# Optimization experiments

Measured on AMD Instinct MI355X. Metric: run time of the kernel, lower is better.

## Reference

```python
import jax, jax.numpy as jnp
import numpy as np

NUM_HEADS = 12
KEEP_RATE = 0.7
EPS = 1e-5  # torch nn.LayerNorm default


def layernorm(x, w, b):
    m = x.mean(-1, keepdims=True)
    v = ((x - m) ** 2).mean(-1, keepdims=True)
    return (x - m) * jax.lax.rsqrt(v + EPS) * w + b


def complement_idx(idx, dim):
    # idx: (B, L) top-k indices into [0, dim). Returns (B, dim-L) sorted complement,
    # matching EViT's scatter-zeros-then-sort trick.
    a = jnp.broadcast_to(jnp.arange(dim, dtype=idx.dtype), idx.shape[:-1] + (dim,))
    masked = jax.vmap(lambda ar, ix: ar.at[ix].set(0))(a, idx)
    n_idx = idx.shape[-1]
    return jnp.sort(masked, axis=-1)[..., n_idx:]


def setup_inputs() -> dict:
    key = jax.random.key(0)
    ks = jax.random.split(key, 8)
    B, N, C = 128, 197, 768
    H = 4 * C
    std = 0.02
    return {
        "x": jax.random.normal(ks[0], (B, N, C), jnp.float32),
        "norm1_w": jnp.ones((C,), jnp.float32),
        "norm1_b": jnp.zeros((C,), jnp.float32),
        "qkv_w": jax.random.normal(ks[1], (C, 3 * C), jnp.float32) * std,  # qkv_bias=False
        "proj_w": jax.random.normal(ks[2], (C, C), jnp.float32) * std,
        "proj_b": jnp.zeros((C,), jnp.float32),
        "norm2_w": jnp.ones((C,), jnp.float32),
        "norm2_b": jnp.zeros((C,), jnp.float32),
        "fc1_w": jax.random.normal(ks[3], (C, H), jnp.float32) * std,
        "fc1_b": jnp.zeros((H,), jnp.float32),
        "fc2_w": jax.random.normal(ks[4], (H, C), jnp.float32) * std,
        "fc2_b": jnp.zeros((C,), jnp.float32),
    }


def reference(x, norm1_w, norm1_b, qkv_w, proj_w, proj_b,
              norm2_w, norm2_b, fc1_w, fc1_b, fc2_w, fc2_b):
    B, N, C = x.shape
    h = NUM_HEADS
    d = C // h
    scale = d ** -0.5

    # ---- Attention (eval mode, no dropout) ----
    xn = layernorm(x, norm1_w, norm1_b)
    qkv = (xn @ qkv_w).reshape(B, N, 3, h, d).transpose(2, 0, 3, 1, 4)
    q, k, v = qkv[0], qkv[1], qkv[2]  # (B, h, N, d)
    attn = jax.nn.softmax(jnp.einsum('bhqd,bhkd->bhqk', q, k) * scale, axis=-1)
    out = jnp.einsum('bhqk,bhkd->bhqd', attn, v).transpose(0, 2, 1, 3).reshape(B, N, C)
    x = x + (out @ proj_w + proj_b)

    # ---- Top-k token selection (keep_rate < 1) ----
    left = int(np.ceil(KEEP_RATE * (N - 1)))          # 138 kept patch tokens
    cls_attn = attn[:, :, 0, 1:].mean(axis=1)         # (B, N-1)
    _, idx = jax.lax.top_k(cls_attn, left)            # sorted descending, like torch.topk
    compl = complement_idx(idx, N - 1)                # (B, M), M = N-1-left

    non_cls = x[:, 1:]                                # (B, N-1, C)
    gather = lambda arr, ix: jnp.take_along_axis(arr, ix[..., None], axis=1)

    x_others = gather(non_cls, idx)                   # (B, L, C)
    non_topk = gather(non_cls, compl)                 # (B, M, C)
    xo_n = x_others / jnp.linalg.norm(x_others, axis=-1, keepdims=True)
    nt_n = non_topk / jnp.linalg.norm(non_topk, axis=-1, keepdims=True)
    distance = jnp.einsum('bmc,blc->bml', nt_n, xo_n)  # cosine similarity (B, M, L)

    # attention-weighted merge of pruned tokens into nearest kept token
    non_cls_w = non_cls * cls_attn[..., None]
    x_others = gather(non_cls_w, idx)
    non_topk = gather(non_cls_w, compl)
    topk_attn = jnp.take_along_axis(cls_attn, idx, axis=1)       # (B, L)
    non_topk_attn = jnp.take_along_axis(cls_attn, compl, axis=1)  # (B, M)
    node_idx = jnp.argmax(distance, axis=-1)                      # (B, M)

    topk_attn = jax.vmap(lambda t, ni, nt: t.at[ni].add(nt))(topk_attn, node_idx, non_topk_attn)
    x_others = jax.vmap(lambda xo, ni, nt: xo.at[ni].add(nt))(x_others, node_idx, non_topk)
    x_others = x_others / topk_attn[..., None]

    x = jnp.concatenate([x[:, :1], x_others], axis=1)  # (B, L+1, C)

    # ---- MLP ----
    xn2 = layernorm(x, norm2_w, norm2_b)
    hmid = jax.nn.gelu(xn2 @ fc1_w + fc1_b, approximate=False)
    x = x + (hmid @ fc2_w + fc2_b)
    return x
```

## Files before the change

### kernel.cpp

```cpp
#include <hip/hip_runtime.h>
#include <math.h>

#define B_ 128
#define N_ 197
#define C_ 768
#define H_ 12
#define D_ 64
#define KEEP_ 138
#define COMP_ 58
#define NOUT_ 139
#define HID_ 3072

typedef __attribute__((ext_vector_type(8))) short bf16x8;
typedef __attribute__((ext_vector_type(8))) _Float16 f16x8;
typedef __attribute__((ext_vector_type(4))) float f32x4;
typedef unsigned short us;

__device__ inline us f2bf(float f) {
    unsigned u = __float_as_uint(f);
    unsigned r = (u + 0x7FFFu + ((u >> 16) & 1u)) >> 16;
    return (us)r;
}
__device__ inline float bf2f(us h) { return __uint_as_float(((unsigned)h) << 16); }
__device__ inline void gload_lds16(const void* g, void* l) {
    __builtin_amdgcn_global_load_lds((const __attribute__((address_space(1))) void*)g,
                                     (__attribute__((address_space(3))) void*)l, 16, 0, 0);
}
__device__ inline void split3(float v, us& h1, us& h2, us& h3) {
    h1 = f2bf(v);
    float r1 = v - bf2f(h1);
    h2 = f2bf(r1);
    h3 = f2bf(r1 - bf2f(h2));
}
__device__ inline void split2h(float v, us& h1, us& h2) {
    float av = fabsf(v);
    float v1 = (av < 6.103515625e-05f) ? 0.f : v;
    _Float16 a = (_Float16)v1;
    float r = (v - (float)a) * 4096.0f;
    _Float16 b = (_Float16)r;
    h1 = *reinterpret_cast<us*>(&a);
    h2 = *reinterpret_cast<us*>(&b);
}

__device__ inline float fast_gelu(float v) {
    float x = v * 0.70710678118654752f;
    float ax = fabsf(x);
    float t = __frcp_rn(__fmaf_rn(0.3275911f, ax, 1.0f));
    float p = __fmaf_rn(1.061405429f, t, -1.453152027f);
    p = __fmaf_rn(p, t, 1.421413741f);
    p = __fmaf_rn(p, t, -0.284496736f);
    p = __fmaf_rn(p, t, 0.254829592f);
    p = p * t;
    float e = __expf(-x * x);
    float erfa = __fmaf_rn(-p, e, 1.0f);
    float er = (x < 0.f) ? -erfa : erfa;
    return 0.5f * v * (1.0f + er);
}

#define WAITV(n) asm volatile("s_waitcnt vmcnt(" #n ")" ::: "memory")
#define RBAR __builtin_amdgcn_s_barrier()

__global__ __launch_bounds__(256) void ln_split2h_kernel(const float* __restrict__ x,
                                                         const float* __restrict__ w,
                                                         const float* __restrict__ bias,
                                                         us* __restrict__ y1,
                                                         us* __restrict__ y2) {
    int row = blockIdx.x;
    const float* xr = x + (size_t)row * C_;
    int tid = threadIdx.x;
    float v[3];
    float s = 0.f, sq = 0.f;
#pragma unroll
    for (int i = 0; i < 3; i++) {
        v[i] = xr[tid + i * 256];
        s += v[i];
        sq += v[i] * v[i];
    }
    __shared__ float s1[256], s2[256];
    s1[tid] = s; s2[tid] = sq;
    __syncthreads();
    for (int o = 128; o > 0; o >>= 1) {
        if (tid < o) { s1[tid] += s1[tid + o]; s2[tid] += s2[tid + o]; }
        __syncthreads();
    }
    float mean = s1[0] * (1.0f / C_);
    float var = s2[0] * (1.0f / C_) - mean * mean;
    float rstd = rsqrtf(var + 1e-5f);
#pragma unroll
    for (int i = 0; i < 3; i++) {
        int c = tid + i * 256;
        float y = (v[i] - mean) * rstd * w[c] + bias[c];
        us h1, h2;
        split2h(y, h1, h2);
        size_t o = (size_t)row * C_ + c;
        y1[o] = h1; y2[o] = h2;
    }
}

__global__ __launch_bounds__(256) void ln2bf_kernel(const float* __restrict__ x,
                                                    const float* __restrict__ w,
                                                    const float* __restrict__ bias,
                                                    us* __restrict__ y) {
    int row = blockIdx.x;
    const float* xr = x + (size_t)row * C_;
    us* yr = y + (size_t)row * C_;
    int tid = threadIdx.x;
    float v[3];
    float s = 0.f, sq = 0.f;
#pragma unroll
    for (int i = 0; i < 3; i++) {
        v[i] = xr[tid + i * 256];
        s += v[i];
        sq += v[i] * v[i];
    }
    __shared__ float s1[256], s2[256];
    s1[tid] = s; s2[tid] = sq;
    __syncthreads();
    for (int o = 128; o > 0; o >>= 1) {
        if (tid < o) { s1[tid] += s1[tid + o]; s2[tid] += s2[tid + o]; }
        __syncthreads();
    }
    float mean = s1[0] * (1.0f / C_);
    float var = s2[0] * (1.0f / C_) - mean * mean;
    float rstd = rsqrtf(var + 1e-5f);
#pragma unroll
    for (int i = 0; i < 3; i++) {
        int c = tid + i * 256;
        yr[c] = f2bf((v[i] - mean) * rstd * w[c] + bias[c]);
    }
}

__global__ __launch_bounds__(256) void wtrans_kernel(const float* __restrict__ in,
                                                     us* __restrict__ out,
                                                     int K, int N) {
    __shared__ float T[32][33];
    int n0 = blockIdx.x * 32, k0 = blockIdx.y * 32;
    int tx = threadIdx.x & 31, ty = threadIdx.x >> 5;
    for (int i = 0; i < 32; i += 8)
        T[ty + i][tx] = in[(size_t)(k0 + ty + i) * N + n0 + tx];
    __syncthreads();
    for (int i = 0; i < 32; i += 8)
        out[(size_t)(n0 + ty + i) * K + k0 + tx] = f2bf(T[tx][ty + i]);
}

__global__ __launch_bounds__(256) void wtrans_split2h_kernel(const float* __restrict__ in,
                                                             us* __restrict__ o1,
                                                             us* __restrict__ o2,
                                                             int K, int N) {
    __shared__ float T[32][33];
    int n0 = blockIdx.x * 32, k0 = blockIdx.y * 32;
    int tx = threadIdx.x & 31, ty = threadIdx.x >> 5;
    for (int i = 0; i < 32; i += 8)
        T[ty + i][tx] = in[(size_t)(k0 + ty + i) * N + n0 + tx];
    __syncthreads();
    for (int i = 0; i < 32; i += 8) {
        us h1, h2;
        split2h(T[tx][ty + i], h1, h2);
        size_t o = (size_t)(n0 + ty + i) * K + k0 + tx;
        o1[o] = h1; o2[o] = h2;
    }
}

template <bool BIAS, bool RES>
__global__ __launch_bounds__(256, 2) void bgemm3h_kernel(const us* __restrict__ A1,
                                                         const us* __restrict__ A2,
                                                         const us* __restrict__ B1,
                                                         const us* __restrict__ B2,
                                                         const float* __restrict__ bias,
                                                         const float* __restrict__ res,
                                                         float* __restrict__ Cm,
                                                         int M, int N, int K) {
    __shared__ short As[2][128 * 64];
    __shared__ short Bs[2][128 * 64];
    int tid = threadIdx.x;
    int lane = tid & 63, wid = tid >> 6;
    int wr = wid >> 1, wc = wid & 1;
    int lr = lane & 15, g = lane >> 4;
    int brow = blockIdx.y * 128, bcol = blockIdx.x * 128;

    f32x4 acc0[4][4] = {};
    f32x4 acc1[4][4] = {};

    for (int k0 = 0; k0 < K; k0 += 64) {
#pragma unroll
        for (int v = 0; v < 4; v++) {
            int rowb = v * 32 + wid * 8;
            int r = rowb + (lane >> 3);
            int slot = lane & 7;
            int chunk = slot ^ (r & 7);
            int garow = brow + r; if (garow >= M) garow = M - 1;
            int gbrow = bcol + r;
            gload_lds16(A1 + (size_t)garow * K + k0 + chunk * 8, &As[0][rowb * 64]);
            gload_lds16(A2 + (size_t)garow * K + k0 + chunk * 8, &As[1][rowb * 64]);
            gload_lds16(B1 + (size_t)gbrow * K + k0 + chunk * 8, &Bs[0][rowb * 64]);
            gload_lds16(B2 + (size_t)gbrow * K + k0 + chunk * 8, &Bs[1][rowb * 64]);
        }
        __syncthreads();
#pragma unroll
        for (int kk = 0; kk < 2; kk++) {
            f16x8 af[2][4], bfr[2][4];
#pragma unroll
            for (int fi = 0; fi < 4; fi++) {
                int ra = wr * 64 + fi * 16 + lr;
                int sla = (kk * 4 + g) ^ (ra & 7);
                int rb = wc * 64 + fi * 16 + lr;
                int slb = (kk * 4 + g) ^ (rb & 7);
#pragma unroll
                for (int s = 0; s < 2; s++) {
                    af[s][fi] = *reinterpret_cast<const f16x8*>(&As[s][ra * 64 + sla * 8]);
                    bfr[s][fi] = *reinterpret_cast<const f16x8*>(&Bs[s][rb * 64 + slb * 8]);
                }
            }
#pragma unroll
            for (int fi = 0; fi < 4; fi++)
#pragma unroll
                for (int fj = 0; fj < 4; fj++) {
                    acc0[fi][fj] = __builtin_amdgcn_mfma_f32_16x16x32_f16(af[0][fi], bfr[0][fj], acc0[fi][fj], 0, 0, 0);
                    acc1[fi][fj] = __builtin_amdgcn_mfma_f32_16x16x32_f16(af[0][fi], bfr[1][fj], acc1[fi][fj], 0, 0, 0);
                    acc1[fi][fj] = __builtin_amdgcn_mfma_f32_16x16x32_f16(af[1][fi], bfr[0][fj], acc1[fi][fj], 0, 0, 0);
                }
        }
        __syncthreads();
    }
#pragma unroll
    for (int fi = 0; fi < 4; fi++) {
#pragma unroll
        for (int fj = 0; fj < 4; fj++) {
            int col = bcol + wc * 64 + fj * 16 + lr;
            float bv = BIAS ? bias[col] : 0.f;
#pragma unroll
            for (int i = 0; i < 4; i++) {
                int r = brow + wr * 64 + fi * 16 + g * 4 + i;
                if (r < M) {
                    float vv = acc0[fi][fj][i] + acc1[fi][fj][i] * (1.0f / 4096.0f) + bv;
                    if (RES) vv += res[(size_t)r * N + col];
                    Cm[(size_t)r * N + col] = vv;
                }
            }
        }
    }
}

template <bool GELU_, bool OUTBF, bool RES>
__global__ __launch_bounds__(256, 4) void bgemm_kernel(const us* __restrict__ A,
                                                       const us* __restrict__ Bt,
                                                       const float* __restrict__ bias,
                                                       const float* __restrict__ res,
                                                       void* __restrict__ Cout,
                                                       int M, int N, int K) {
    __shared__ short As0[128 * 32];
    __shared__ short Bs0[128 * 32];
    __shared__ short As1[128 * 32];
    __shared__ short Bs1[128 * 32];
    int tid = threadIdx.x;
    int lane = tid & 63, wid = tid >> 6;
    int wr = wid >> 1, wc = wid & 1;
    int lr = lane & 15, g = lane >> 4;
    int brow = blockIdx.y * 128, bcol = blockIdx.x * 128;
    int lrow = lane >> 2, lslot = lane & 3;
    const int sa = (g ^ ((lr >> 1) & 3)) * 8;

    f32x4 acc[4][4] = {};

    auto stage = [&](short (&Aa)[128 * 32], short (&Bb)[128 * 32], int k0) {
#pragma unroll
        for (int v = 0; v < 2; v++) {
            int rowb = wid * 32 + v * 16;
            int ra = rowb + lrow;
            int hsel = (lslot ^ ((lrow >> 1) & 3)) * 8;
            int garow = brow + ra; if (garow >= M) garow = M - 1;
            gload_lds16(A + (size_t)garow * K + k0 + hsel, &Aa[rowb * 32]);
            gload_lds16(Bt + (size_t)(bcol + ra) * K + k0 + hsel, &Bb[rowb * 32]);
        }
    };
    auto compute = [&](short (&Aa)[128 * 32], short (&Bb)[128 * 32]) {
        bf16x8 af[4], bfr[4];
#pragma unroll
        for (int fi = 0; fi < 4; fi++)
            af[fi] = *reinterpret_cast<const bf16x8*>(&Aa[(wr * 64 + fi * 16 + lr) * 32 + sa]);
#pragma unroll
        for (int fj = 0; fj < 4; fj++)
            bfr[fj] = *reinterpret_cast<const bf16x8*>(&Bb[(wc * 64 + fj * 16 + lr) * 32 + sa]);
#pragma unroll
        for (int fi = 0; fi < 4; fi++)
#pragma unroll
            for (int fj = 0; fj < 4; fj++)
                acc[fi][fj] = __builtin_amdgcn_mfma_f32_16x16x32_bf16(af[fi], bfr[fj], acc[fi][fj], 0, 0, 0);
    };

    stage(As0, Bs0, 0);
    for (int k0 = 0; k0 < K; k0 += 64) {
        if (k0 + 32 < K) {
            stage(As1, Bs1, k0 + 32);
            WAITV(4);
        } else {
            WAITV(0);
        }
        RBAR;
        compute(As0, Bs0);
        RBAR;
        if (k0 + 64 < K) {
            stage(As0, Bs0, k0 + 64);
            WAITV(4);
        } else {
            WAITV(0);
        }
        RBAR;
        compute(As1, Bs1);
        RBAR;
    }
#pragma unroll
    for (int fi = 0; fi < 4; fi++) {
#pragma unroll
        for (int fj = 0; fj < 4; fj++) {
            int col = bcol + wc * 64 + fj * 16 + lr;
            float bv = bias[col];
#pragma unroll
            for (int i = 0; i < 4; i++) {
                int r = brow + wr * 64 + fi * 16 + g * 4 + i;
                if (r < M) {
                    float vv = acc[fi][fj][i] + bv;
                    if (GELU_) vv = fast_gelu(vv);
                    if (OUTBF) {
                        ((us*)Cout)[(size_t)r * N + col] = f2bf(vv);
                    } else {
                        if (RES) vv += res[(size_t)r * N + col];
                        ((float*)Cout)[(size_t)r * N + col] = vv;
                    }
                }
            }
        }
    }
}

__global__ __launch_bounds__(512, 1) void attn11_kernel(const float* __restrict__ qkv,
                                                        us* __restrict__ ao1,
                                                        us* __restrict__ ao2,
                                                        float* __restrict__ attn0,
                                                        int b0) {
    int hh = blockIdx.x, b = blockIdx.y;
    int tid = threadIdx.x, lane = tid & 63, wv = tid >> 6;
    int lr = lane & 15, g = lane >> 4;
    __shared__ short Ks[3][208 * 64];
    __shared__ short Vt[2][64 * 224];
    __shared__ unsigned Pscr[8][16 * 32];
    const size_t base = (size_t)b * N_ * 3 * C_ + (size_t)hh * D_;

    for (int i = tid; i < 208 * 8; i += 512) {
        int k = i >> 3, oct = i & 7;
        int d0 = (oct ^ (k & 7)) * 8;
        float tv[8];
        if (k < N_) {
            const float4* kp = reinterpret_cast<const float4*>(qkv + base + (size_t)k * 3 * C_ + C_ + d0);
            float4 aa = kp[0], bb = kp[1];
            tv[0] = aa.x; tv[1] = aa.y; tv[2] = aa.z; tv[3] = aa.w;
            tv[4] = bb.x; tv[5] = bb.y; tv[6] = bb.z; tv[7] = bb.w;
        } else {
#pragma unroll
            for (int e = 0; e < 8; e++) tv[e] = 0.f;
        }
        bf16x8 h1v, h2v, h3v;
#pragma unroll
        for (int e = 0; e < 8; e++) {
            us ha, hb, hc;
            split3(tv[e], ha, hb, hc);
            h1v[e] = (short)ha; h2v[e] = (short)hb; h3v[e] = (short)hc;
        }
        int di = k * 64 + oct * 8;
        *reinterpret_cast<bf16x8*>(&Ks[0][di]) = h1v;
        *reinterpret_cast<bf16x8*>(&Ks[1][di]) = h2v;
        *reinterpret_cast<bf16x8*>(&Ks[2][di]) = h3v;
    }
    {
        int d = tid & 63, jb = tid >> 6;
        for (int it = 0; it < 28; it++) {
            int k = it * 8 + jb;
            float vv = (k < N_) ? qkv[base + (size_t)k * 3 * C_ + 2 * C_ + d] : 0.f;
            us p1 = f2bf(vv);
            us p2 = f2bf(vv - bf2f(p1));
            int idx = d * 224 + (((k >> 3) ^ (d & 3)) * 8) + (k & 7);
            Vt[0][idx] = (short)p1;
            Vt[1][idx] = (short)p2;
        }
    }
    __syncthreads();

#pragma unroll
    for (int chunk = 0; chunk < 2; chunk++) {
        int qbase = chunk * 128 + wv * 16;
        bf16x8 qf1[2], qf2[2], qf3[2];
        int qrow = qbase + lr;
#pragma unroll
        for (int kk = 0; kk < 2; kk++) {
            float qv[8];
            if (qrow < N_) {
                const float4* qp = reinterpret_cast<const float4*>(qkv + base + (size_t)qrow * 3 * C_ + kk * 32 + g * 8);
                float4 aa = qp[0], bb = qp[1];
                qv[0] = aa.x; qv[1] = aa.y; qv[2] = aa.z; qv[3] = aa.w;
                qv[4] = bb.x; qv[5] = bb.y; qv[6] = bb.z; qv[7] = bb.w;
            } else {
#pragma unroll
                for (int e = 0; e < 8; e++) qv[e] = 0.f;
            }
#pragma unroll
            for (int e = 0; e < 8; e++) {
                us ha, hb, hc;
                split3(qv[e], ha, hb, hc);
                qf1[kk][e] = (short)ha; qf2[kk][e] = (short)hb; qf3[kk][e] = (short)hc;
            }
        }
        f32x4 sacc[13] = {};
#pragma unroll
        for (int kt = 0; kt < 13; kt++) {
#pragma unroll
            for (int kk = 0; kk < 2; kk++) {
                int row = kt * 16 + lr;
                int sl = ((kk * 4 + g) ^ (row & 7)) * 8;
                const bf16x8 b1 = *reinterpret_cast<const bf16x8*>(&Ks[0][row * 64 + sl]);
                const bf16x8 b2 = *reinterpret_cast<const bf16x8*>(&Ks[1][row * 64 + sl]);
                const bf16x8 b3 = *reinterpret_cast<const bf16x8*>(&Ks[2][row * 64 + sl]);
                sacc[kt] = __builtin_amdgcn_mfma_f32_16x16x32_bf16(qf1[kk], b1, sacc[kt], 0, 0, 0);
                sacc[kt] = __builtin_amdgcn_mfma_f32_16x16x32_bf16(qf1[kk], b2, sacc[kt], 0, 0, 0);
                sacc[kt] = __builtin_amdgcn_mfma_f32_16x16x32_bf16(qf2[kk], b1, sacc[kt], 0, 0, 0);
                sacc[kt] = __builtin_amdgcn_mfma_f32_16x16x32_bf16(qf1[kk], b3, sacc[kt], 0, 0, 0);
                sacc[kt] = __builtin_amdgcn_mfma_f32_16x16x32_bf16(qf3[kk], b1, sacc[kt], 0, 0, 0);
                sacc[kt] = __builtin_amdgcn_mfma_f32_16x16x32_bf16(qf2[kk], b2, sacc[kt], 0, 0, 0);
            }
        }
#pragma unroll
        for (int i = 0; i < 4; i++) {
            float m = -1e30f;
#pragma unroll
            for (int kt = 0; kt < 13; kt++) {
                int k = kt * 16 + lr;
                float lgv = (k < N_) ? sacc[kt][i] * 0.125f : -1e30f;
                sacc[kt][i] = lgv;
                m = fmaxf(m, lgv);
            }
            m = fmaxf(m, __shfl_xor(m, 1, 64));
            m = fmaxf(m, __shfl_xor(m, 2, 64));
            m = fmaxf(m, __shfl_xor(m, 4, 64));
            m = fmaxf(m, __shfl_xor(m, 8, 64));
            float se = 0.f;
#pragma unroll
            for (int kt = 0; kt < 13; kt++) {
                int k = kt * 16 + lr;
                float e = (k < N_) ? expf(sacc[kt][i] - m) : 0.f;
                sacc[kt][i] = e;
                se += e;
            }
            se += __shfl_xor(se, 1, 64);
            se += __shfl_xor(se, 2, 64);
            se += __shfl_xor(se, 4, 64);
            se += __shfl_xor(se, 8, 64);
            float inv = 1.0f / se;
#pragma unroll
            for (int kt = 0; kt < 13; kt++) sacc[kt][i] *= inv;
        }
        if (chunk == 0 && wv == 0 && g == 0) {
#pragma unroll
            for (int kt = 0; kt < 13; kt++) {
                int k = kt * 16 + lr;
                if (k < N_) attn0[((size_t)(b0 + b) * H_ + hh) * N_ + k] = sacc[kt][0];
            }
        }
        f32x4 oacc[4] = {};
#pragma unroll
        for (int sect = 0; sect < 7; sect++) {
#pragma unroll
            for (int t = 0; t < 2; t++) {
                int kt = sect * 2 + t;
#pragma unroll
                for (int i = 0; i < 4; i++) {
                    float p = (kt < 13) ? sacc[kt][i] : 0.f;
                    us h1 = f2bf(p);
                    us h2 = f2bf(p - bf2f(h1));
                    Pscr[wv][(g * 4 + i) * 32 + t * 16 + lr] = (unsigned)h1 | ((unsigned)h2 << 16);
                }
            }
            uint4 u0 = *reinterpret_cast<const uint4*>(&Pscr[wv][lr * 32 + g * 8]);
            uint4 u1 = *reinterpret_cast<const uint4*>(&Pscr[wv][lr * 32 + g * 8 + 4]);
            unsigned uu[8] = {u0.x, u0.y, u0.z, u0.w, u1.x, u1.y, u1.z, u1.w};
            bf16x8 pa1, pa2;
#pragma unroll
            for (int e = 0; e < 8; e++) {
                pa1[e] = (short)(uu[e] & 0xffffu);
                pa2[e] = (short)(uu[e] >> 16);
            }
#pragma unroll
            for (int dt = 0; dt < 4; dt++) {
                int row = dt * 16 + lr;
                int cc = sect * 4 + g;
                int idx = row * 224 + ((cc ^ (row & 3)) * 8);
                const bf16x8 v1 = *reinterpret_cast<const bf16x8*>(&Vt[0][idx]);
                const bf16x8 v2 = *reinterpret_cast<const bf16x8*>(&Vt[1][idx]);
                oacc[dt] = __builtin_amdgcn_mfma_f32_16x16x32_bf16(pa1, v1, oacc[dt], 0, 0, 0);
                oacc[dt] = __builtin_amdgcn_mfma_f32_16x16x32_bf16(pa1, v2, oacc[dt], 0, 0, 0);
                oacc[dt] = __builtin_amdgcn_mfma_f32_16x16x32_bf16(pa2, v1, oacc[dt], 0, 0, 0);
            }
        }
#pragma unroll
        for (int dt = 0; dt < 4; dt++) {
#pragma unroll
            for (int i = 0; i < 4; i++) {
                int q = qbase + g * 4 + i;
                if (q < N_) {
                    int d = dt * 16 + lr;
                    size_t oi = ((size_t)(b * N_ + q)) * C_ + (size_t)hh * D_ + d;
                    us h1, h2;
                    split2h(oacc[dt][i], h1, h2);
                    ao1[oi] = h1; ao2[oi] = h2;
                }
            }
        }
    }
}

__global__ __launch_bounds__(256) void cls_kernel(const float* __restrict__ attn0,
                                                  float* __restrict__ cls) {
    int b = blockIdx.x, tid = threadIdx.x;
    if (tid < N_ - 1) {
        float s = 0.f;
        for (int hh = 0; hh < H_; hh++) s += attn0[((size_t)b * H_ + hh) * N_ + 1 + tid];
        cls[b * (N_ - 1) + tid] = s * (1.0f / H_);
    }
}

__global__ __launch_bounds__(256) void topk_kernel(const float* __restrict__ cls,
                                                   int* __restrict__ idx,
                                                   int* __restrict__ cmp) {
    int b = blockIdx.x, tid = threadIdx.x;
    __shared__ float vals[196];
    __shared__ int rk[196];
    if (tid < 196) vals[tid] = cls[b * 196 + tid];
    __syncthreads();
    if (tid < 196) {
        float v = vals[tid];
        int r = 0;
        for (int j = 0; j < 196; j++) {
            float u = vals[j];
            r += (u > v) || (u == v && j < tid);
        }
        rk[tid] = r;
    }
    __syncthreads();
    if (tid < 196) {
        int r = rk[tid];
        if (r < KEEP_) {
            idx[b * KEEP_ + r] = tid;
        } else {
            int pos = 0;
            for (int j = 0; j < tid; j++) pos += (rk[j] >= KEEP_);
            cmp[b * COMP_ + pos] = tid;
        }
    }
}

__global__ __launch_bounds__(256) void rnorm_kernel(const float* __restrict__ x1,
                                                    float* __restrict__ rn) {
    int i = blockIdx.x, b = blockIdx.y, tid = threadIdx.x;
    const float* xr = x1 + ((size_t)b * N_ + 1 + i) * C_;
    float sq = 0.f;
#pragma unroll
    for (int k = 0; k < 3; k++) {
        float v = xr[tid + k * 256];
        sq += v * v;
    }
    __shared__ float s2[256];
    s2[tid] = sq;
    __syncthreads();
    for (int o = 128; o > 0; o >>= 1) {
        if (tid < o) s2[tid] += s2[tid + o];
        __syncthreads();
    }
    if (tid == 0) rn[b * 196 + i] = rsqrtf(s2[0]);
}

__global__ __launch_bounds__(256, 3) void dist3_kernel(const float* __restrict__ x1,
                                                       const float* __restrict__ rn,
                                                       const int* __restrict__ idx,
                                                       const int* __restrict__ cmp,
                                                       int* __restrict__ node) {
    int b = blockIdx.x, half = blockIdx.y;
    int l0 = half * 29;
    int tid = threadIdx.x;
    __shared__ __align__(16) float As2[64][36];
    __shared__ float Bs2[64][161];
    __shared__ int cpl[29];
    __shared__ int til[KEEP_];
    __shared__ float rnt[KEEP_];
    if (tid < 29) cpl[tid] = cmp[b * COMP_ + l0 + tid];
    if (tid < KEEP_) {
        int t = idx[b * KEEP_ + tid];
        til[tid] = t;
        rnt[tid] = rn[b * 196 + t];
    }
    __syncthreads();
    int tr = tid >> 5, tc = tid & 31;
    float acc[4][5] = {};
    for (int k0 = 0; k0 < C_; k0 += 64) {
        for (int ii = tid; ii < 29 * 64; ii += 256) {
            int l = ii >> 6, k = ii & 63;
            As2[k][l] = x1[((size_t)b * N_ + 1 + cpl[l]) * C_ + k0 + k];
        }
        for (int ii = tid; ii < KEEP_ * 64; ii += 256) {
            int m = ii >> 6, k = ii & 63;
            Bs2[k][m] = x1[((size_t)b * N_ + 1 + til[m]) * C_ + k0 + k];
        }
        __syncthreads();
#pragma unroll 4
        for (int k = 0; k < 64; k++) {
            float ar[4], br[5];
            *reinterpret_cast<float4*>(ar) = *reinterpret_cast<const float4*>(&As2[k][tr * 4]);
#pragma unroll
            for (int j = 0; j < 5; j++) br[j] = Bs2[k][tc * 5 + j];
#pragma unroll
            for (int i = 0; i < 4; i++)
#pragma unroll
                for (int j = 0; j < 5; j++) acc[i][j] += ar[i] * br[j];
        }
        __syncthreads();
    }
#pragma unroll
    for (int i = 0; i < 4; i++) {
        int ll = tr * 4 + i;
        if (ll < 29) {
            float best = -3.0e38f;
            int bm = 0x7fffffff;
#pragma unroll
            for (int j = 0; j < 5; j++) {
                int m = tc * 5 + j;
                if (m < KEEP_) {
                    float dv = acc[i][j] * rnt[m];
                    if (dv > best) { best = dv; bm = m; }
                }
            }
            for (int o = 1; o < 32; o <<= 1) {
                float ov = __shfl_xor(best, o, 64);
                int oi = __shfl_xor(bm, o, 64);
                if (ov > best || (ov == best && oi < bm)) { best = ov; bm = oi; }
            }
            if (tc == 0) node[b * COMP_ + l0 + ll] = bm;
        }
    }
}

__global__ __launch_bounds__(256) void fuse_kernel(const float* __restrict__ x1,
                                                   const float* __restrict__ cls,
                                                   const int* __restrict__ idx,
                                                   const int* __restrict__ cmp,
                                                   const int* __restrict__ node,
                                                   float* __restrict__ x2) {
    int mr = blockIdx.x, b = blockIdx.y, tid = threadIdx.x;
    if (mr == 0) {
        for (int c = tid; c < C_; c += 256)
            x2[(size_t)b * NOUT_ * C_ + c] = x1[(size_t)b * N_ * C_ + c];
        return;
    }
    int m = mr - 1;
    __shared__ int nds[COMP_];
    __shared__ int cps[COMP_];
    if (tid < COMP_) {
        nds[tid] = node[b * COMP_ + tid];
        cps[tid] = cmp[b * COMP_ + tid];
    }
    __syncthreads();
    int ti = idx[b * KEEP_ + m];
    float ta = cls[b * 196 + ti];
    float denom = ta;
    for (int l = 0; l < COMP_; l++)
        if (nds[l] == m) denom += cls[b * 196 + cps[l]];
    float a[3];
    const float* xr = x1 + ((size_t)b * N_ + 1 + ti) * C_;
#pragma unroll
    for (int i = 0; i < 3; i++) a[i] = xr[tid + i * 256] * ta;
    for (int l = 0; l < COMP_; l++) {
        if (nds[l] == m) {
            float ca = cls[b * 196 + cps[l]];
            const float* yr = x1 + ((size_t)b * N_ + 1 + cps[l]) * C_;
#pragma unroll
            for (int i = 0; i < 3; i++) a[i] += yr[tid + i * 256] * ca;
        }
    }
    float invd = 1.0f / denom;
#pragma unroll
    for (int i = 0; i < 3; i++)
        x2[((size_t)b * NOUT_ + mr) * C_ + tid + i * 256] = a[i] * invd;
}

extern "C" void kernel_launch(void* const* d_in, const int* in_sizes, int n_in,
                              void* d_out, int out_size, void* d_ws, size_t ws_size,
                              hipStream_t stream) {
    const float* x       = (const float*)d_in[0];
    const float* norm1_w = (const float*)d_in[1];
    const float* norm1_b = (const float*)d_in[2];
    const float* qkv_w   = (const float*)d_in[3];
    const float* proj_w  = (const float*)d_in[4];
    const float* proj_b  = (const float*)d_in[5];
    const float* norm2_w = (const float*)d_in[6];
    const float* norm2_b = (const float*)d_in[7];
    const float* fc1_w   = (const float*)d_in[8];
    const float* fc1_b   = (const float*)d_in[9];
    const float* fc2_w   = (const float*)d_in[10];
    const float* fc2_b   = (const float*)d_in[11];
    float* out = (float*)d_out;

    const int M1 = B_ * N_;
    const int M2 = B_ * NOUT_;
    const size_t WT_F  = 2359296;
    const size_t C3C   = (size_t)C_ * 3 * C_;
    const size_t CC    = (size_t)C_ * C_;

    const size_t small_f = (size_t)B_ * H_ * N_ + 2u * B_ * 196;
    const size_t small_i = (size_t)B_ * KEEP_ + 2u * B_ * COMP_;
    const size_t x1_f = (size_t)M1 * C_;

    const int cb_t[4] = {64, 32, 16, 4};
    const int rm_t[4] = {M2, M2, 4864, 320};
    int CB = 4, RMLP = 320;
    size_t scr_f = 0;
    {
        bool ok = false;
        for (int tier = 0; tier < 4; tier++) {
            int cb = cb_t[tier], rm = rm_t[tier];
            size_t cbnc = (size_t)cb * N_ * C_;
            size_t front_f = (C3C + CC) + cbnc + 3 * cbnc;
            size_t mlp_f   = WT_F + (size_t)rm * 1920;
            size_t sf      = front_f > mlp_f ? front_f : mlp_f;
            size_t nd      = (x1_f + sf + small_f) * 4 + small_i * 4;
            if (ws_size >= nd) { CB = cb; RMLP = rm; scr_f = sf; ok = true; break; }
        }
        if (!ok) return;
    }

    float* ws = (float*)d_ws;
    float* x1    = ws;
    float* scr   = x1 + x1_f;
    float* attn0 = scr + scr_f;
    float* cls   = attn0 + (size_t)B_ * H_ * N_;
    float* rn    = cls + B_ * 196;
    int* idxb    = (int*)(rn + B_ * 196);
    int* cmpb    = idxb + B_ * KEEP_;
    int* nodeb   = cmpb + B_ * COMP_;
    float* x2    = out;

    const size_t cbnc = (size_t)CB * N_ * C_;
    us* sb  = (us*)scr;
    us* qw1 = sb;            us* qw2 = qw1 + C3C;
    us* pw1 = qw2 + C3C;     us* pw2 = pw1 + CC;
    us* xn1 = pw2 + CC;      us* xn2 = xn1 + cbnc;
    float* qkv_c = (float*)(xn2 + cbnc);
    us* ao1 = xn1;  us* ao2 = xn2;
    us* fc1wt  = (us*)scr;
    us* fc2wt  = fc1wt + (size_t)C_ * HID_;
    us* xn2bf  = fc2wt + (size_t)C_ * HID_;
    us* hmidbf = xn2bf + (size_t)RMLP * C_;

    wtrans_split2h_kernel<<<dim3(3 * C_ / 32, C_ / 32), 256, 0, stream>>>(qkv_w, qw1, qw2, C_, 3 * C_);
    wtrans_split2h_kernel<<<dim3(C_ / 32, C_ / 32), 256, 0, stream>>>(proj_w, pw1, pw2, C_, C_);

    for (int b0 = 0; b0 < B_; b0 += CB) {
        int cb = (B_ - b0 < CB) ? (B_ - b0) : CB;
        int Mc = cb * N_;
        const float* xch = x + (size_t)b0 * N_ * C_;
        ln_split2h_kernel<<<Mc, 256, 0, stream>>>(xch, norm1_w, norm1_b, xn1, xn2);
        bgemm3h_kernel<false, false><<<dim3(3 * C_ / 128, (Mc + 127) / 128), 256, 0, stream>>>(
            xn1, xn2, qw1, qw2, nullptr, nullptr, qkv_c, Mc, 3 * C_, C_);
        attn11_kernel<<<dim3(H_, cb), 512, 0, stream>>>(qkv_c, ao1, ao2, attn0, b0);
        bgemm3h_kernel<true, true><<<dim3(C_ / 128, (Mc + 127) / 128), 256, 0, stream>>>(
            ao1, ao2, pw1, pw2, proj_b, xch, x1 + (size_t)b0 * N_ * C_, Mc, C_, C_);
    }

    cls_kernel<<<B_, 256, 0, stream>>>(attn0, cls);
    topk_kernel<<<B_, 256, 0, stream>>>(cls, idxb, cmpb);
    rnorm_kernel<<<dim3(196, B_), 256, 0, stream>>>(x1, rn);
    dist3_kernel<<<dim3(B_, 2), 256, 0, stream>>>(x1, rn, idxb, cmpb, nodeb);
    fuse_kernel<<<dim3(NOUT_, B_), 256, 0, stream>>>(x1, cls, idxb, cmpb, nodeb, x2);

    wtrans_kernel<<<dim3(HID_ / 32, C_ / 32), 256, 0, stream>>>(fc1_w, fc1wt, C_, HID_);
    wtrans_kernel<<<dim3(C_ / 32, HID_ / 32), 256, 0, stream>>>(fc2_w, fc2wt, HID_, C_);

    for (int r0 = 0; r0 < M2; r0 += RMLP) {
        int R = M2 - r0 < RMLP ? M2 - r0 : RMLP;
        ln2bf_kernel<<<R, 256, 0, stream>>>(x2 + (size_t)r0 * C_, norm2_w, norm2_b, xn2bf);
        bgemm_kernel<true, true, false><<<dim3(HID_ / 128, (R + 127) / 128), 256, 0, stream>>>(
            xn2bf, fc1wt, fc1_b, nullptr, hmidbf, R, HID_, C_);
        bgemm_kernel<false, false, true><<<dim3(C_ / 128, (R + 127) / 128), 256, 0, stream>>>(
            hmidbf, fc2wt, fc2_b, x2 + (size_t)r0 * C_, out + (size_t)r0 * C_, R, C_, HID_);
    }
}
```

Measured before the change: 1.433 ms.

## Replace double-buffered K=32 staging with single-buffered K=64 tile in bf16 GEMM

The bf16 GEMM main loop drops its two 32-wide LDS buffers with staggered prefetch and vmcnt waits. It now loads a single 64-wide K tile per iteration, using a new XOR swizzle over 8 chunks, and brackets the compute with __syncthreads. This halves the number of barriers per 64 K elements and simplifies the loop, but it removes the overlap of global loads with MFMA compute. Loads now fully stall before each compute step.

Result: faster. 1.382 ms (-3.5%).

```diff
diff --git a/kernel.cpp b/kernel.cpp
--- a/kernel.cpp
+++ b/kernel.cpp
@@ -248,66 +248,47 @@
                                                        const float* __restrict__ res,
                                                        void* __restrict__ Cout,
                                                        int M, int N, int K) {
-    __shared__ short As0[128 * 32];
-    __shared__ short Bs0[128 * 32];
-    __shared__ short As1[128 * 32];
-    __shared__ short Bs1[128 * 32];
+    __shared__ short As[128 * 64];
+    __shared__ short Bs[128 * 64];
     int tid = threadIdx.x;
     int lane = tid & 63, wid = tid >> 6;
     int wr = wid >> 1, wc = wid & 1;
     int lr = lane & 15, g = lane >> 4;
     int brow = blockIdx.y * 128, bcol = blockIdx.x * 128;
-    int lrow = lane >> 2, lslot = lane & 3;
-    const int sa = (g ^ ((lr >> 1) & 3)) * 8;
 
     f32x4 acc[4][4] = {};
 
-    auto stage = [&](short (&Aa)[128 * 32], short (&Bb)[128 * 32], int k0) {
-#pragma unroll
-        for (int v = 0; v < 2; v++) {
-            int rowb = wid * 32 + v * 16;
-            int ra = rowb + lrow;
-            int hsel = (lslot ^ ((lrow >> 1) & 3)) * 8;
-            int garow = brow + ra; if (garow >= M) garow = M - 1;
-            gload_lds16(A + (size_t)garow * K + k0 + hsel, &Aa[rowb * 32]);
-            gload_lds16(Bt + (size_t)(bcol + ra) * K + k0 + hsel, &Bb[rowb * 32]);
-        }
-    };
-    auto compute = [&](short (&Aa)[128 * 32], short (&Bb)[128 * 32]) {
-        bf16x8 af[4], bfr[4];
-#pragma unroll
-        for (int fi = 0; fi < 4; fi++)
-            af[fi] = *reinterpret_cast<const bf16x8*>(&Aa[(wr * 64 + fi * 16 + lr) * 32 + sa]);
-#pragma unroll
-        for (int fj = 0; fj < 4; fj++)
-            bfr[fj] = *reinterpret_cast<const bf16x8*>(&Bb[(wc * 64 + fj * 16 + lr) * 32 + sa]);
-#pragma unroll
-        for (int fi = 0; fi < 4; fi++)
-#pragma unroll
-            for (int fj = 0; fj < 4; fj++)
-                acc[fi][fj] = __builtin_amdgcn_mfma_f32_16x16x32_bf16(af[fi], bfr[fj], acc[fi][fj], 0, 0, 0);
-    };
-
-    stage(As0, Bs0, 0);
     for (int k0 = 0; k0 < K; k0 += 64) {
-        if (k0 + 32 < K) {
-            stage(As1, Bs1, k0 + 32);
-            WAITV(4);
-        } else {
-            WAITV(0);
-        }
-        RBAR;
-        compute(As0, Bs0);
-        RBAR;
-        if (k0 + 64 < K) {
-            stage(As0, Bs0, k0 + 64);
-            WAITV(4);
-        } else {
-            WAITV(0);
-        }
-        RBAR;
-        compute(As1, Bs1);
-        RBAR;
+#pragma unroll
+        for (int v = 0; v < 4; v++) {
+            int rowb = v * 32 + wid * 8;
+            int r = rowb + (lane >> 3);
+            int slot = lane & 7;
+            int chunk = slot ^ (r & 7);
+            int garow = brow + r; if (garow >= M) garow = M - 1;
+            gload_lds16(A + (size_t)garow * K + k0 + chunk * 8, &As[rowb * 64]);
+            gload_lds16(Bt + (size_t)(bcol + r) * K + k0 + chunk * 8, &Bs[rowb * 64]);
+        }
+        __syncthreads();
+#pragma unroll
+        for (int kk = 0; kk < 2; kk++) {
+            bf16x8 af[4], bfr[4];
+#pragma unroll
+            for (int fi = 0; fi < 4; fi++) {
+                int ra = wr * 64 + fi * 16 + lr;
+                int sla = (kk * 4 + g) ^ (ra & 7);
+                int rb = wc * 64 + fi * 16 + lr;
+                int slb = (kk * 4 + g) ^ (rb & 7);
+                af[fi] = *reinterpret_cast<const bf16x8*>(&As[ra * 64 + sla * 8]);
+                bfr[fi] = *reinterpret_cast<const bf16x8*>(&Bs[rb * 64 + slb * 8]);
+            }
+#pragma unroll
+            for (int fi = 0; fi < 4; fi++)
+#pragma unroll
+                for (int fj = 0; fj < 4; fj++)
+                    acc[fi][fj] = __builtin_amdgcn_mfma_f32_16x16x32_bf16(af[fi], bfr[fj], acc[fi][fj], 0, 0, 0);
+        }
+        __syncthreads();
     }
 #pragma unroll
     for (int fi = 0; fi < 4; fi++) {
```
